# Kernel tuning notes

Measured on AMD Instinct MI355X. Metric: run time of the kernel, lower is better.

Reference implementation:

```python
import jax, jax.numpy as jnp
import numpy as np

# --- GLIF3 / AlphaPSC constants (from NeuronParam / NetworkConfig) ---
N = 2048            # n_neuron
NE = int(N * 0.8)   # excitatory count = 1638
NUM_IN_NEU = 1024
NUM_OUT_NEU = 128
T, B, NUM_IN, NUM_OUT = 100, 64, 784, 10
V_TH, V_RESET = -45.0, -60.0
C_M, TAU = 2.0, 20.0
K_ASC, ASC_AMP = 1.0 / 80.0, -0.2
TAU_REF, BASE_I = 2.0, 0.12
DT = 1.0


def _spike(x):
    # heaviside spike (Erf surrogate only matters for backward)
    return (x >= 0).astype(x.dtype)


def setup_inputs() -> dict:
    key = jax.random.key(0)
    k1, k2, k3, k4 = jax.random.split(key, 4)
    x = jax.random.normal(k1, (T, B, NUM_IN), jnp.float32)
    W_in = jax.random.normal(k2, (NUM_IN_NEU, NUM_IN), jnp.float32) / np.sqrt(NUM_IN)
    W_rec = jax.random.normal(k3, (N, N), jnp.float32) * (5.0 / np.sqrt(N))  # rec_weight_scaling
    W_out = jax.random.normal(k4, (NUM_OUT, NUM_OUT_NEU), jnp.float32) / np.sqrt(NUM_OUT_NEU)
    # replicate NetworkConfig.__post_init__ index sampling (same RandomState, same order)
    rand = np.random.RandomState(32)
    input_indices = jnp.asarray(rand.choice(NE, NUM_IN_NEU, replace=False), jnp.int32)
    output_indices = jnp.asarray(rand.choice(NE, NUM_OUT_NEU, replace=False), jnp.int32)
    tau_syn = jnp.concatenate([jnp.full((NE,), 5.8, jnp.float32),
                               jnp.full((N - NE,), 6.5, jnp.float32)])
    return dict(x=x, W_in=W_in, W_rec=W_rec, W_out=W_out, tau_syn=tau_syn,
                input_indices=input_indices, output_indices=output_indices)


def _run(x, W_in, W_rec, W_out, tau_syn, input_indices, output_indices, spike_fn):
    Tn, Bn, _ = x.shape
    # input projection then scatter into the excitatory input subset
    proj = jnp.einsum('tbi,ni->tbn', x, W_in)                   # (T, B, num_input_neuron)
    inp = jnp.zeros((Tn, Bn, N), x.dtype).at[..., input_indices].set(proj)
    d_syn = jnp.exp(-DT / tau_syn)                              # (N,) per-neuron alpha decay
    e_tau = jnp.e / tau_syn                                     # alpha-kernel peak normalization
    d_asc = jnp.exp(-K_ASC * DT)

    def step(carry, inp_t):
        v, psc, rise, asc, ref, spk = carry
        # recurrent connection + external drive feeds the alpha synapse
        I_in = spk @ W_rec.T + inp_t                            # (B, N)
        psc_n = d_syn * (psc + DT * rise)                       # alpha-PSC (dual-exp) update
        rise_n = d_syn * rise + e_tau * I_in
        asc_n = d_asc * asc + ASC_AMP * spk                     # after-spike current
        active = (ref <= 0).astype(v.dtype)                     # refractory gate
        dv = (psc_n + asc_n + BASE_I) / C_M - (v - V_RESET) / TAU
        v_n = v + active * DT * dv
        spk_n = spike_fn(v_n - V_TH) * active
        v_n = v_n - spk_n * (V_TH - V_RESET)                    # soft reset (hard_reset=False)
        ref_n = jnp.where(spk_n > 0, TAU_REF, jnp.maximum(ref - DT, 0.0))
        return (v_n, psc_n, rise_n, asc_n, ref_n, spk_n), spk_n

    z = jnp.zeros((Bn, N), x.dtype)
    c0 = (jnp.full((Bn, N), V_RESET, x.dtype), z, z, z, z, z)
    _, spikes = jax.lax.scan(step, c0, inp)                     # spikes: (T, B, N)
    rate = spikes[..., output_indices].mean(axis=0)             # (B, num_output_neuron)
    return rate @ W_out.T                                       # (B, num_output)


def reference(x, W_in, W_rec, W_out, tau_syn, input_indices, output_indices):
    return _run(x, W_in, W_rec, W_out, tau_syn, input_indices, output_indices, _spike)
```

## Files before the change

### kernel.cpp

```cpp
#include <hip/hip_runtime.h>
#include <math.h>

#define N_NEU    2048
#define BB       64
#define TT       100
#define KIN      784
#define NIN_NEU  1024
#define N_OUT    10
#define NOUT_NEU 128

typedef unsigned int u32;
typedef unsigned long long u64;
typedef unsigned short u16;
typedef double f64x4 __attribute__((ext_vector_type(4)));

__global__ void k_prep(const float* __restrict__ tau, double* __restrict__ d_syn,
                       double* __restrict__ e_tau, int* __restrict__ inv){
    int n = blockIdx.x * blockDim.x + threadIdx.x;
    if(n < N_NEU){
        double tv = (double)tau[n];
        d_syn[n] = exp(-1.0 / tv);
        e_tau[n] = 2.718281828459045 / tv;
        inv[n] = -1;
    }
}

__global__ void k_scatter(const int* __restrict__ idx, int* __restrict__ inv){
    int j = blockIdx.x * blockDim.x + threadIdx.x;
    if(j < NIN_NEU) inv[idx[j]] = j;
}

__global__ void k_zero(u64* __restrict__ exch, int nexch){
    int j = blockIdx.x * blockDim.x + threadIdx.x;
    if(j < nexch) exch[j] = 0ull;
}

__global__ void k_probe(int* __restrict__ flag){
    int l = threadIdx.x & 63;
    double a = (double)((l & 15)*4 + (l >> 4) + 1);
    double b = (double)((l >> 4)*16 + (l & 15) + 1);
    f64x4 acc = {0.0, 0.0, 0.0, 0.0};
    acc = __builtin_amdgcn_mfma_f64_16x16x4f64(a, b, acc, 0, 0, 0);
    bool oka = true, okb = true;
    int j = l & 15;
    #pragma unroll
    for(int r=0;r<4;r++){
        int ia = 4*(l >> 4) + r;
        int ib = (l >> 4) + 4*r;
        double expA = 0.0, expB = 0.0;
        #pragma unroll
        for(int k=0;k<4;k++){
            expA += (double)((4*ia + k + 1) * (16*k + j + 1));
            expB += (double)((4*ib + k + 1) * (16*k + j + 1));
        }
        oka = oka && (acc[r] == expA);
        okb = okb && (acc[r] == expB);
    }
    bool alla = __all(oka), allb = __all(okb);
    if(threadIdx.x == 0) *flag = alla ? 0 : (allb ? 1 : 2);
}

__global__ __launch_bounds__(256) void k_tr(const float* __restrict__ Wrec, float* __restrict__ Wt){
    __shared__ float tile[32][33];
    int bx = blockIdx.x, by = blockIdx.y;
    int txx = threadIdx.x, tyy = threadIdx.y;
    #pragma unroll
    for(int j=0;j<4;j++)
        tile[tyy+8*j][txx] = Wrec[(size_t)(by*32 + tyy+8*j)*N_NEU + bx*32 + txx];
    __syncthreads();
    #pragma unroll
    for(int j=0;j<4;j++)
        Wt[(size_t)(bx*32 + tyy+8*j)*N_NEU + by*32 + txx] = tile[txx][tyy+8*j];
}

__global__ __launch_bounds__(256) void k_proj_mfma(const float* __restrict__ X, const float* __restrict__ Win,
                                                   const int* __restrict__ flagp, double* __restrict__ projC){
    const int flag = *flagp;
    if(flag >= 2) return;
    __shared__ float As[32][81];
    __shared__ float Bs[32][81];
    const int t   = blockIdx.x;
    const int c0  = blockIdx.y * 64;
    const int tid = threadIdx.x;
    const int w   = tid >> 6;
    const int l   = tid & 63;
    const int g   = l >> 4;
    const int cl  = l & 15;
    const int lr  = tid >> 2;
    const int lk  = (tid & 3) * 8;

    f64x4 acc[4] = {{0.,0.,0.,0.},{0.,0.,0.,0.},{0.,0.,0.,0.},{0.,0.,0.,0.}};

    for(int k0 = 0; k0 < KIN; k0 += 32){
        int kk = k0 + lk;
        float a8[8], b8[8];
        if(kk + 8 <= KIN){
            const float* pa = X   + (size_t)(t*64 + lr)*KIN + kk;
            const float* pb = Win + (size_t)(c0 + lr)*KIN + kk;
            float4 ra0 = *reinterpret_cast<const float4*>(pa);
            float4 ra1 = *reinterpret_cast<const float4*>(pa + 4);
            float4 rb0 = *reinterpret_cast<const float4*>(pb);
            float4 rb1 = *reinterpret_cast<const float4*>(pb + 4);
            a8[0]=ra0.x; a8[1]=ra0.y; a8[2]=ra0.z; a8[3]=ra0.w;
            a8[4]=ra1.x; a8[5]=ra1.y; a8[6]=ra1.z; a8[7]=ra1.w;
            b8[0]=rb0.x; b8[1]=rb0.y; b8[2]=rb0.z; b8[3]=rb0.w;
            b8[4]=rb1.x; b8[5]=rb1.y; b8[6]=rb1.z; b8[7]=rb1.w;
        } else {
            #pragma unroll
            for(int e=0;e<8;e++){ a8[e]=0.0f; b8[e]=0.0f; }
        }
        #pragma unroll
        for(int e=0;e<8;e++){ As[lk+e][lr] = a8[e]; Bs[lk+e][lr] = b8[e]; }
        __syncthreads();

        #pragma unroll
        for(int kq=0;kq<8;kq++){
            double a = (double)As[kq*4 + g][w*16 + cl];
            #pragma unroll
            for(int ct=0;ct<4;ct++){
                double bb = (double)Bs[kq*4 + g][ct*16 + cl];
                acc[ct] = __builtin_amdgcn_mfma_f64_16x16x4f64(a, bb, acc[ct], 0, 0, 0);
            }
        }
        __syncthreads();
    }

    #pragma unroll
    for(int ct=0;ct<4;ct++){
        int c = c0 + ct*16 + cl;
        #pragma unroll
        for(int j=0;j<4;j++){
            int b = w*16 + ((flag == 0) ? (4*g + j) : (g + 4*j));
            projC[((size_t)b*TT + t)*NIN_NEU + c] = acc[ct][j];
        }
    }
}

__global__ __launch_bounds__(256) void k_proj_valu(const float* __restrict__ X, const float* __restrict__ Win,
                                                   const int* __restrict__ flagp, double* __restrict__ projC){
    if(*flagp < 2) return;
    __shared__ float As[32][68];
    __shared__ float Bs[32][68];
    const int r0 = blockIdx.x * 64;
    const int c0 = blockIdx.y * 64;
    const int t  = threadIdx.x;
    const int lr = t >> 2;
    const int lk = (t & 3) * 8;
    const int tx = t & 15, ty = t >> 4;
    double acc[4][4] = {};
    for(int k0 = 0; k0 < KIN; k0 += 32){
        int kk = k0 + lk;
        float a8[8], b8[8];
        if(kk + 8 <= KIN){
            const float* pa = X   + (size_t)(r0+lr)*KIN + kk;
            const float* pb = Win + (size_t)(c0+lr)*KIN + kk;
            float4 ra0 = *reinterpret_cast<const float4*>(pa);
            float4 ra1 = *reinterpret_cast<const float4*>(pa + 4);
            float4 rb0 = *reinterpret_cast<const float4*>(pb);
            float4 rb1 = *reinterpret_cast<const float4*>(pb + 4);
            a8[0]=ra0.x; a8[1]=ra0.y; a8[2]=ra0.z; a8[3]=ra0.w;
            a8[4]=ra1.x; a8[5]=ra1.y; a8[6]=ra1.z; a8[7]=ra1.w;
            b8[0]=rb0.x; b8[1]=rb0.y; b8[2]=rb0.z; b8[3]=rb0.w;
            b8[4]=rb1.x; b8[5]=rb1.y; b8[6]=rb1.z; b8[7]=rb1.w;
        } else {
            #pragma unroll
            for(int e=0;e<8;e++){ a8[e]=0.0f; b8[e]=0.0f; }
        }
        #pragma unroll
        for(int e=0;e<8;e++){ As[lk+e][lr] = a8[e]; Bs[lk+e][lr] = b8[e]; }
        __syncthreads();
        #pragma unroll
        for(int kkk=0;kkk<32;kkk++){
            float4 af = *reinterpret_cast<const float4*>(&As[kkk][ty*4]);
            float4 bf = *reinterpret_cast<const float4*>(&Bs[kkk][tx*4]);
            double a[4] = {(double)af.x,(double)af.y,(double)af.z,(double)af.w};
            double b[4] = {(double)bf.x,(double)bf.y,(double)bf.z,(double)bf.w};
            #pragma unroll
            for(int i=0;i<4;i++)
                #pragma unroll
                for(int j=0;j<4;j++)
                    acc[i][j] += a[i]*b[j];
        }
        __syncthreads();
    }
    const int tt = blockIdx.x;
    #pragma unroll
    for(int j=0;j<4;j++){
        int c = c0 + tx*4 + j;
        #pragma unroll
        for(int i=0;i<4;i++){
            int b = ty*4 + i;
            projC[((size_t)b*TT + tt)*NIN_NEU + c] = acc[i][j];
        }
    }
}

__global__ __launch_bounds__(256) void k_sim(
        const double* __restrict__ projC, const float* __restrict__ Wt,
        const double* __restrict__ dsyn, const double* __restrict__ etau,
        const int* __restrict__ inv,
        u64* __restrict__ exch, double* __restrict__ cntout){
    __shared__ double Ip[4][256];
    __shared__ u32 words[64];
    __shared__ u16 list[N_NEU];
    __shared__ int cntS;

    const int bid = blockIdx.x;
    const int b   = bid >> 3;
    const int q   = bid & 7;
    const int tid = threadIdx.x;
    const int n   = q*256 + tid;
    const int team = tid >> 6;
    const int c4   = (tid & 63) * 4;
    const float*  WtQ   = Wt + q*256;
    const double* projB = projC + (size_t)b*TT*NIN_NEU;

    u64* myE = exch + (size_t)bid*32;

    const double ds = dsyn[n], et = etau[n];
    const int jv = inv[n];
    const double dasc = exp(-0.0125);
    double v=-60.0, psc=0.0, rise=0.0, asc=0.0, ref=0.0, spk=0.0, creg=0.0;

    if(tid == 0) cntS = 0;
    __syncthreads();

    for(int t=0;t<TT;t++){
        double pp = (jv >= 0) ? projB[(size_t)t*NIN_NEU + jv] : 0.0;

        const int cc  = cntS;
        const int beg = (cc * team)     >> 2;
        const int end = (cc * (team+1)) >> 2;
        double I[4] = {0.0, 0.0, 0.0, 0.0};
        int i = beg;
        for(; i + 8 <= end; i += 8){
            int m[8];
            #pragma unroll
            for(int u=0;u<8;u++) m[u] = list[i+u];
            float4 wv[8];
            #pragma unroll
            for(int u=0;u<8;u++)
                wv[u] = *reinterpret_cast<const float4*>(WtQ + ((size_t)m[u] << 11) + c4);
            #pragma unroll
            for(int u=0;u<8;u++){
                I[0] += (double)wv[u].x; I[1] += (double)wv[u].y;
                I[2] += (double)wv[u].z; I[3] += (double)wv[u].w;
            }
        }
        for(; i < end; ++i){
            int mm = list[i];
            float4 w4 = *reinterpret_cast<const float4*>(WtQ + ((size_t)mm << 11) + c4);
            I[0] += (double)w4.x; I[1] += (double)w4.y;
            I[2] += (double)w4.z; I[3] += (double)w4.w;
        }
        #pragma unroll
        for(int u=0;u<4;u++) Ip[team][c4+u] = I[u];
        __syncthreads();

        double Irec = Ip[0][tid] + Ip[1][tid] + Ip[2][tid] + Ip[3][tid] + pp;

        double psc_n  = ds * (psc + rise);
        double rise_n = ds * rise + et * Irec;
        double asc_n  = dasc * asc + (-0.2) * spk;
        double act    = (ref <= 0.0) ? 1.0 : 0.0;
        double dv  = (psc_n + asc_n + 0.12) / 2.0 - (v - (-60.0)) / 20.0;
        double v_n = v + act * dv;
        double s_n = ((v_n - (-45.0)) >= 0.0) ? act : 0.0;
        v_n = v_n - s_n * 15.0;
        double ref_n = (s_n > 0.0) ? 2.0 : fmax(ref - 1.0, 0.0);
        v = v_n; psc = psc_n; rise = rise_n; asc = asc_n; ref = ref_n; spk = s_n;
        creg += s_n;

        u64 bal = __ballot(s_n > 0.0);
        int w = tid >> 6, lane = tid & 63;
        u64 tagv = ((u64)(t+1)) << 32;
        if(lane == 0){
            u32 lo = (u32)bal, hi = (u32)(bal >> 32);
            words[q*8 + 2*w]     = lo;
            words[q*8 + 2*w + 1] = hi;
            u64* dst = myE + (size_t)(t & 1)*16;
            atomicExch(&dst[2*w],     tagv | (u64)lo);
            atomicExch(&dst[2*w + 1], tagv | (u64)hi);
        }
        if(tid < 56){
            int pidx = tid >> 3;
            int w2   = tid & 7;
            int q2   = pidx + (pidx >= q ? 1 : 0);
            u64* src = exch + (size_t)(b*8 + q2)*32 + (size_t)(t & 1)*16;
            u64 val = atomicAdd(&src[w2], 0ull);
            while((val >> 32) != (u64)(t+1)){
                __builtin_amdgcn_s_sleep(1);
                val = atomicAdd(&src[w2], 0ull);
            }
            words[q2*8 + w2] = (u32)val;
        }
        __syncthreads();

        if(tid < 64){
            u32 wv = words[tid];
            int c = __popc(wv);
            int incl = c;
            #pragma unroll
            for(int off=1; off<64; off<<=1){
                int x = __shfl_up(incl, off);
                if(tid >= off) incl += x;
            }
            int excl = incl - c;
            u32 z = wv;
            int base = tid * 32;
            while(z){
                int bp = __ffs(z) - 1;
                z &= z - 1;
                list[excl++] = (u16)(base + bp);
            }
            if(tid == 63) cntS = incl;
        }
        __syncthreads();
    }

    cntout[(size_t)b*N_NEU + n] = creg;
}

__global__ void k_final(const double* __restrict__ cnt, const int* __restrict__ oidx,
                        const float* __restrict__ Wout, float* __restrict__ out){
    int i = blockIdx.x * blockDim.x + threadIdx.x;
    if(i >= BB * N_OUT) return;
    int b = i / N_OUT, o = i - b * N_OUT;
    double accv = 0.0;
    for(int j=0;j<NOUT_NEU;j++){
        double rate = cnt[(size_t)b*N_NEU + oidx[j]] / 100.0;
        accv += rate * (double)Wout[o*NOUT_NEU + j];
    }
    out[i] = (float)accv;
}

extern "C" void kernel_launch(void* const* d_in, const int* in_sizes, int n_in,
                              void* d_out, int out_size, void* d_ws, size_t ws_size,
                              hipStream_t stream){
    const float* X    = (const float*)d_in[0];
    const float* Win  = (const float*)d_in[1];
    const float* Wrec = (const float*)d_in[2];
    const float* Wout = (const float*)d_in[3];
    const float* tau  = (const float*)d_in[4];
    const int*   iidx = (const int*)d_in[5];
    const int*   oidx = (const int*)d_in[6];
    float* out = (float*)d_out;

    char* w = (char*)d_ws;
    const size_t OFF_PROJ = 0;
    const size_t OFF_CNT  = OFF_PROJ + (size_t)BB*TT*NIN_NEU*8;
    const size_t OFF_WT   = OFF_CNT + (size_t)BB*N_NEU*8;
    const size_t OFF_EXCH = OFF_WT + (size_t)N_NEU*N_NEU*4;
    const size_t OFF_DS   = OFF_EXCH + 131072;
    const size_t OFF_ET   = OFF_DS + N_NEU*8;
    const size_t OFF_INV  = OFF_ET + N_NEU*8;
    const size_t OFF_FLAG = OFF_INV + N_NEU*4;

    double* projC = (double*)(w + OFF_PROJ);
    double* cnt   = (double*)(w + OFF_CNT);
    float*  Wt    = (float*)(w + OFF_WT);
    u64*    exch  = (u64*)(w + OFF_EXCH);
    double* dsyn  = (double*)(w + OFF_DS);
    double* etau  = (double*)(w + OFF_ET);
    int*    inv   = (int*)(w + OFF_INV);
    int*    flag  = (int*)(w + OFF_FLAG);

    k_prep     <<<dim3(8),      dim3(256),  0, stream>>>(tau, dsyn, etau, inv);
    k_scatter  <<<dim3(4),      dim3(256),  0, stream>>>(iidx, inv);
    k_zero     <<<dim3(64),     dim3(256),  0, stream>>>(exch, 16384);
    k_probe    <<<dim3(1),      dim3(64),   0, stream>>>(flag);
    k_tr       <<<dim3(64,64),  dim3(32,8), 0, stream>>>(Wrec, Wt);
    k_proj_mfma<<<dim3(100,16), dim3(256),  0, stream>>>(X, Win, flag, projC);
    k_proj_valu<<<dim3(100,16), dim3(256),  0, stream>>>(X, Win, flag, projC);
    k_sim      <<<dim3(8*BB),   dim3(256),  0, stream>>>(projC, Wt, dsyn, etau, inv, exch, cnt);
    k_final    <<<dim3(3),      dim3(256),  0, stream>>>(cnt, oidx, Wout, out);
}
```

Measured before the change: 578.9 us.

## Process two batch rows per block to halve inter-block spike exchange rounds

Each simulation block now advances two batch elements (b and b+32) in an interleaved loop, so the grid shrinks from 512 to 256 blocks. The spin-wait exchange of spike bitmasks for both batches is merged into one polling phase per timestep, and both spike lists are built in parallel by two wavefronts. The aim is to cut the number of global-memory synchronisation rounds and let the weight gathers of the second batch hide exchange latency. In exchange, each block does twice the gather work per step and only 256 blocks are resident, which may underuse the CUs.

```diff
diff --git a/kernel.cpp b/kernel.cpp
--- a/kernel.cpp
+++ b/kernel.cpp
@@ -201,124 +201,200 @@
         const int* __restrict__ inv,
         u64* __restrict__ exch, double* __restrict__ cntout){
     __shared__ double Ip[4][256];
-    __shared__ u32 words[64];
-    __shared__ u16 list[N_NEU];
-    __shared__ int cntS;
+    __shared__ u32 wordsA[64], wordsB[64];
+    __shared__ u16 listA[N_NEU], listB[N_NEU];
+    __shared__ int cntA, cntB;
 
     const int bid = blockIdx.x;
-    const int b   = bid >> 3;
+    const int bp  = bid >> 3;
     const int q   = bid & 7;
+    const int bA  = bp;
+    const int bEx = bp + 32;
     const int tid = threadIdx.x;
     const int n   = q*256 + tid;
     const int team = tid >> 6;
     const int c4   = (tid & 63) * 4;
     const float*  WtQ   = Wt + q*256;
-    const double* projB = projC + (size_t)b*TT*NIN_NEU;
-
-    u64* myE = exch + (size_t)bid*32;
+    const double* projA = projC + (size_t)bA*TT*NIN_NEU;
+    const double* projB = projC + (size_t)bEx*TT*NIN_NEU;
+
+    u64* myE = exch + (size_t)bid*64;
 
     const double ds = dsyn[n], et = etau[n];
     const int jv = inv[n];
     const double dasc = exp(-0.0125);
-    double v=-60.0, psc=0.0, rise=0.0, asc=0.0, ref=0.0, spk=0.0, creg=0.0;
-
-    if(tid == 0) cntS = 0;
+    double vA=-60.0, pscA=0.0, riseA=0.0, ascA=0.0, refA=0.0, spkA=0.0, cregA=0.0;
+    double vB=-60.0, pscB=0.0, riseB=0.0, ascB=0.0, refB=0.0, spkB=0.0, cregB=0.0;
+
+    if(tid == 0){ cntA = 0; cntB = 0; }
     __syncthreads();
 
     for(int t=0;t<TT;t++){
-        double pp = (jv >= 0) ? projB[(size_t)t*NIN_NEU + jv] : 0.0;
-
-        const int cc  = cntS;
-        const int beg = (cc * team)     >> 2;
-        const int end = (cc * (team+1)) >> 2;
-        double I[4] = {0.0, 0.0, 0.0, 0.0};
-        int i = beg;
-        for(; i + 8 <= end; i += 8){
-            int m[8];
-            #pragma unroll
-            for(int u=0;u<8;u++) m[u] = list[i+u];
-            float4 wv[8];
-            #pragma unroll
-            for(int u=0;u<8;u++)
-                wv[u] = *reinterpret_cast<const float4*>(WtQ + ((size_t)m[u] << 11) + c4);
-            #pragma unroll
-            for(int u=0;u<8;u++){
-                I[0] += (double)wv[u].x; I[1] += (double)wv[u].y;
-                I[2] += (double)wv[u].z; I[3] += (double)wv[u].w;
-            }
-        }
-        for(; i < end; ++i){
-            int mm = list[i];
-            float4 w4 = *reinterpret_cast<const float4*>(WtQ + ((size_t)mm << 11) + c4);
-            I[0] += (double)w4.x; I[1] += (double)w4.y;
-            I[2] += (double)w4.z; I[3] += (double)w4.w;
-        }
-        #pragma unroll
-        for(int u=0;u<4;u++) Ip[team][c4+u] = I[u];
-        __syncthreads();
-
-        double Irec = Ip[0][tid] + Ip[1][tid] + Ip[2][tid] + Ip[3][tid] + pp;
-
-        double psc_n  = ds * (psc + rise);
-        double rise_n = ds * rise + et * Irec;
-        double asc_n  = dasc * asc + (-0.2) * spk;
-        double act    = (ref <= 0.0) ? 1.0 : 0.0;
-        double dv  = (psc_n + asc_n + 0.12) / 2.0 - (v - (-60.0)) / 20.0;
-        double v_n = v + act * dv;
-        double s_n = ((v_n - (-45.0)) >= 0.0) ? act : 0.0;
-        v_n = v_n - s_n * 15.0;
-        double ref_n = (s_n > 0.0) ? 2.0 : fmax(ref - 1.0, 0.0);
-        v = v_n; psc = psc_n; rise = rise_n; asc = asc_n; ref = ref_n; spk = s_n;
-        creg += s_n;
-
-        u64 bal = __ballot(s_n > 0.0);
-        int w = tid >> 6, lane = tid & 63;
-        u64 tagv = ((u64)(t+1)) << 32;
-        if(lane == 0){
-            u32 lo = (u32)bal, hi = (u32)(bal >> 32);
-            words[q*8 + 2*w]     = lo;
-            words[q*8 + 2*w + 1] = hi;
-            u64* dst = myE + (size_t)(t & 1)*16;
-            atomicExch(&dst[2*w],     tagv | (u64)lo);
-            atomicExch(&dst[2*w + 1], tagv | (u64)hi);
-        }
-        if(tid < 56){
-            int pidx = tid >> 3;
-            int w2   = tid & 7;
-            int q2   = pidx + (pidx >= q ? 1 : 0);
-            u64* src = exch + (size_t)(b*8 + q2)*32 + (size_t)(t & 1)*16;
-            u64 val = atomicAdd(&src[w2], 0ull);
-            while((val >> 32) != (u64)(t+1)){
-                __builtin_amdgcn_s_sleep(1);
-                val = atomicAdd(&src[w2], 0ull);
-            }
-            words[q2*8 + w2] = (u32)val;
-        }
-        __syncthreads();
-
-        if(tid < 64){
-            u32 wv = words[tid];
-            int c = __popc(wv);
-            int incl = c;
-            #pragma unroll
-            for(int off=1; off<64; off<<=1){
-                int x = __shfl_up(incl, off);
-                if(tid >= off) incl += x;
-            }
-            int excl = incl - c;
-            u32 z = wv;
-            int base = tid * 32;
-            while(z){
-                int bp = __ffs(z) - 1;
-                z &= z - 1;
-                list[excl++] = (u16)(base + bp);
-            }
-            if(tid == 63) cntS = incl;
-        }
-        __syncthreads();
-    }
-
-    cntout[(size_t)b*N_NEU + n] = creg;
+        const u64 tagv = ((u64)(t+1)) << 32;
+        const int par = t & 1;
+        double ppA = (jv >= 0) ? projA[(size_t)t*NIN_NEU + jv] : 0.0;
+        double ppB = (jv >= 0) ? projB[(size_t)t*NIN_NEU + jv] : 0.0;
+
+        {
+            const int cc  = cntA;
+            const int beg = (cc * team)     >> 2;
+            const int end = (cc * (team+1)) >> 2;
+            double I[4] = {0.0, 0.0, 0.0, 0.0};
+            int i = beg;
+            for(; i + 8 <= end; i += 8){
+                int m[8];
+                #pragma unroll
+                for(int u=0;u<8;u++) m[u] = listA[i+u];
+                float4 wv[8];
+                #pragma unroll
+                for(int u=0;u<8;u++)
+                    wv[u] = *reinterpret_cast<const float4*>(WtQ + ((size_t)m[u] << 11) + c4);
+                #pragma unroll
+                for(int u=0;u<8;u++){
+                    I[0] += (double)wv[u].x; I[1] += (double)wv[u].y;
+                    I[2] += (double)wv[u].z; I[3] += (double)wv[u].w;
+                }
+            }
+            for(; i < end; ++i){
+                int mm = listA[i];
+                float4 w4 = *reinterpret_cast<const float4*>(WtQ + ((size_t)mm << 11) + c4);
+                I[0] += (double)w4.x; I[1] += (double)w4.y;
+                I[2] += (double)w4.z; I[3] += (double)w4.w;
+            }
+            #pragma unroll
+            for(int u=0;u<4;u++) Ip[team][c4+u] = I[u];
+        }
+        __syncthreads();
+        {
+            double Irec = Ip[0][tid] + Ip[1][tid] + Ip[2][tid] + Ip[3][tid] + ppA;
+            double psc_n  = ds * (pscA + riseA);
+            double rise_n = ds * riseA + et * Irec;
+            double asc_n  = dasc * ascA + (-0.2) * spkA;
+            double act    = (refA <= 0.0) ? 1.0 : 0.0;
+            double dv  = (psc_n + asc_n + 0.12) / 2.0 - (vA - (-60.0)) / 20.0;
+            double v_n = vA + act * dv;
+            double s_n = ((v_n - (-45.0)) >= 0.0) ? act : 0.0;
+            v_n = v_n - s_n * 15.0;
+            double ref_n = (s_n > 0.0) ? 2.0 : fmax(refA - 1.0, 0.0);
+            vA = v_n; pscA = psc_n; riseA = rise_n; ascA = asc_n; refA = ref_n; spkA = s_n;
+            cregA += s_n;
+
+            u64 bal = __ballot(s_n > 0.0);
+            int w = tid >> 6, lane = tid & 63;
+            if(lane == 0){
+                u32 lo = (u32)bal, hi = (u32)(bal >> 32);
+                wordsA[q*8 + 2*w]     = lo;
+                wordsA[q*8 + 2*w + 1] = hi;
+                u64* dst = myE + (size_t)par*16;
+                atomicExch(&dst[2*w],     tagv | (u64)lo);
+                atomicExch(&dst[2*w + 1], tagv | (u64)hi);
+            }
+        }
+        __syncthreads();
+
+        {
+            const int cc  = cntB;
+            const int beg = (cc * team)     >> 2;
+            const int end = (cc * (team+1)) >> 2;
+            double I[4] = {0.0, 0.0, 0.0, 0.0};
+            int i = beg;
+            for(; i + 8 <= end; i += 8){
+                int m[8];
+                #pragma unroll
+                for(int u=0;u<8;u++) m[u] = listB[i+u];
+                float4 wv[8];
+                #pragma unroll
+                for(int u=0;u<8;u++)
+                    wv[u] = *reinterpret_cast<const float4*>(WtQ + ((size_t)m[u] << 11) + c4);
+                #pragma unroll
+                for(int u=0;u<8;u++){
+                    I[0] += (double)wv[u].x; I[1] += (double)wv[u].y;
+                    I[2] += (double)wv[u].z; I[3] += (double)wv[u].w;
+                }
+            }
+            for(; i < end; ++i){
+                int mm = listB[i];
+                float4 w4 = *reinterpret_cast<const float4*>(WtQ + ((size_t)mm << 11) + c4);
+                I[0] += (double)w4.x; I[1] += (double)w4.y;
+                I[2] += (double)w4.z; I[3] += (double)w4.w;
+            }
+            #pragma unroll
+            for(int u=0;u<4;u++) Ip[team][c4+u] = I[u];
+        }
+        __syncthreads();
+        {
+            double Irec = Ip[0][tid] + Ip[1][tid] + Ip[2][tid] + Ip[3][tid] + ppB;
+            double psc_n  = ds * (pscB + riseB);
+            double rise_n = ds * riseB + et * Irec;
+            double asc_n  = dasc * ascB + (-0.2) * spkB;
+            double act    = (refB <= 0.0) ? 1.0 : 0.0;
+            double dv  = (psc_n + asc_n + 0.12) / 2.0 - (vB - (-60.0)) / 20.0;
+            double v_n = vB + act * dv;
+            double s_n = ((v_n - (-45.0)) >= 0.0) ? act : 0.0;
+            v_n = v_n - s_n * 15.0;
+            double ref_n = (s_n > 0.0) ? 2.0 : fmax(refB - 1.0, 0.0);
+            vB = v_n; pscB = psc_n; riseB = rise_n; ascB = asc_n; refB = ref_n; spkB = s_n;
+            cregB += s_n;
+
+            u64 bal = __ballot(s_n > 0.0);
+            int w = tid >> 6, lane = tid & 63;
+            if(lane == 0){
+                u32 lo = (u32)bal, hi = (u32)(bal >> 32);
+                wordsB[q*8 + 2*w]     = lo;
+                wordsB[q*8 + 2*w + 1] = hi;
+                u64* dst = myE + 32 + (size_t)par*16;
+                atomicExch(&dst[2*w],     tagv | (u64)lo);
+                atomicExch(&dst[2*w + 1], tagv | (u64)hi);
+            }
+        }
+
+        if(t < TT-1){
+            if(tid < 112){
+                int pidx = tid >> 4;
+                int sub  = tid & 15;
+                int bsel = sub >> 3;
+                int w2   = sub & 7;
+                int q2   = pidx + (pidx >= q ? 1 : 0);
+                u64* src = exch + (size_t)(bp*8 + q2)*64 + (size_t)bsel*32 + (size_t)par*16 + w2;
+                u64 val = atomicAdd(src, 0ull);
+                while((val >> 32) != (u64)(t+1)){
+                    __builtin_amdgcn_s_sleep(1);
+                    val = atomicAdd(src, 0ull);
+                }
+                if(bsel == 0) wordsA[q2*8 + w2] = (u32)val;
+                else          wordsB[q2*8 + w2] = (u32)val;
+            }
+            __syncthreads();
+
+            if(tid < 128){
+                const int lane = tid & 63;
+                const u32 wv = (tid < 64) ? wordsA[lane] : wordsB[lane];
+                int c = __popc(wv);
+                int incl = c;
+                #pragma unroll
+                for(int off=1; off<64; off<<=1){
+                    int x = __shfl_up(incl, off);
+                    if(lane >= off) incl += x;
+                }
+                int excl = incl - c;
+                u32 z = wv;
+                int base = lane * 32;
+                u16* ldst = (tid < 64) ? listA : listB;
+                while(z){
+                    int bp2 = __ffs(z) - 1;
+                    z &= z - 1;
+                    ldst[excl++] = (u16)(base + bp2);
+                }
+                if(lane == 63){
+                    if(tid < 64) cntA = incl; else cntB = incl;
+                }
+            }
+            __syncthreads();
+        }
+    }
+
+    cntout[(size_t)bA*N_NEU + n]  = cregA;
+    cntout[(size_t)bEx*N_NEU + n] = cregB;
 }
 
 __global__ void k_final(const double* __restrict__ cnt, const int* __restrict__ oidx,
@@ -372,6 +448,6 @@
     k_tr       <<<dim3(64,64),  dim3(32,8), 0, stream>>>(Wrec, Wt);
     k_proj_mfma<<<dim3(100,16), dim3(256),  0, stream>>>(X, Win, flag, projC);
     k_proj_valu<<<dim3(100,16), dim3(256),  0, stream>>>(X, Win, flag, projC);
-    k_sim      <<<dim3(8*BB),   dim3(256),  0, stream>>>(projC, Wt, dsyn, etau, inv, exch, cnt);
+    k_sim      <<<dim3(256),    dim3(256),  0, stream>>>(projC, Wt, dsyn, etau, inv, exch, cnt);
     k_final    <<<dim3(3),      dim3(256),  0, stream>>>(cnt, oidx, Wout, out);
 }
```

Measured after the change: 693.2 us. 1.2x slower.
